# Kernel tuning notes

Measured on AMD Instinct MI355X. Metric: run time of the kernel, lower is better.

Reference implementation:

```python
import jax, jax.numpy as jnp
import numpy as np

N_NODES = 50000
N_EDGES = 800000
N_SUPPORTS = 3
F_IN = 128
F_OUT = 128
BATCH = 1


def _spmm(rows_k, cols_k, vals_k, sup, n_nodes):
    # sup: [B, N, F] dense features; sparse adj given as COO (rows, cols, vals)
    # out[b, r, :] += vals * sup[b, c, :]
    gathered = sup[:, cols_k, :] * vals_k[None, :, None]  # [B, E, F]
    seg = jax.vmap(lambda g: jax.ops.segment_sum(g, rows_k, num_segments=n_nodes))
    return seg(gathered)  # [B, N, F]


def setup_inputs() -> dict:
    key = jax.random.key(0)
    k1, k2, k3, k4, k5 = jax.random.split(key, 5)
    x = jax.random.normal(k1, (BATCH, N_NODES, F_IN), dtype=jnp.float32)
    rows = jax.random.randint(k2, (N_SUPPORTS, N_EDGES), 0, N_NODES)
    cols = jax.random.randint(k3, (N_SUPPORTS, N_EDGES), 0, N_NODES)
    vals = jax.random.uniform(k4, (N_SUPPORTS, N_EDGES), dtype=jnp.float32)
    kernels = jax.random.normal(k5, (N_SUPPORTS, F_IN, F_OUT), dtype=jnp.float32) * (2.0 / (F_IN + F_OUT)) ** 0.5
    bias = jnp.zeros((F_OUT,), dtype=jnp.float32)
    return {"x": x, "rows": rows, "cols": cols, "vals": vals, "kernels": kernels, "bias": bias}


def reference(x, rows, cols, vals, kernels, bias):
    n_nodes = x.shape[1]
    out = None
    for k in range(kernels.shape[0]):  # small fixed number of Chebyshev supports
        sup = jnp.einsum('bnf,fo->bno', x, kernels[k])  # dense feature transform
        acc = _spmm(rows[k], cols[k], vals[k], sup, n_nodes)
        out = acc if out is None else out + acc
    out = out + bias  # bias broadcast over [B, N, F_OUT]
    return jax.nn.relu(out)
```

## Files before the change

### kernel.cpp

```cpp
#include <hip/hip_runtime.h>

#define N_NODES 50000
#define N_EDGES 800000
#define N_SUP   3
#define FD      128
#define NP_PAD  50176

#define NB      196
#define RPB     256
#define EPB     3125
#define NBLK_E  256

typedef __attribute__((ext_vector_type(8))) short bf16x8;
typedef __attribute__((ext_vector_type(4))) float f32x4;

__device__ __forceinline__ unsigned rtn_bf16(float f) {
    unsigned u = __float_as_uint(f);
    return (u + 0x7FFFu + ((u >> 16) & 1u)) >> 16;
}
__device__ __forceinline__ float bf_lo(unsigned g) { return __uint_as_float(g << 16); }
__device__ __forceinline__ float bf_hi(unsigned g) { return __uint_as_float(g & 0xFFFF0000u); }

__global__ __launch_bounds__(256) void cvt_x_kernel(const float4* __restrict__ x4,
                                                    uint2* __restrict__ xb) {
    int i = blockIdx.x * 256 + threadIdx.x;
    if (i >= N_NODES * 32) return;
    float4 v = x4[i];
    xb[i] = make_uint2(rtn_bf16(v.x) | (rtn_bf16(v.y) << 16),
                       rtn_bf16(v.z) | (rtn_bf16(v.w) << 16));
}

__global__ __launch_bounds__(256) void cvt_w_kernel(const float* __restrict__ W,
                                                    uint4* __restrict__ wtb) {
    int tid = blockIdx.x * 256 + threadIdx.x;
    if (tid >= 128 * 48) return;
    int col = tid / 48, p = tid % 48;
    int qlog = (p & ~3) | ((p & 3) ^ ((col >> 1) & 3));
    int k0 = qlog * 8;
    unsigned w0 = rtn_bf16(W[(k0 + 0) * 128 + col]) | (rtn_bf16(W[(k0 + 1) * 128 + col]) << 16);
    unsigned w1 = rtn_bf16(W[(k0 + 2) * 128 + col]) | (rtn_bf16(W[(k0 + 3) * 128 + col]) << 16);
    unsigned w2 = rtn_bf16(W[(k0 + 4) * 128 + col]) | (rtn_bf16(W[(k0 + 5) * 128 + col]) << 16);
    unsigned w3 = rtn_bf16(W[(k0 + 6) * 128 + col]) | (rtn_bf16(W[(k0 + 7) * 128 + col]) << 16);
    wtb[col * 48 + p] = make_uint4(w0, w1, w2, w3);
}

__global__ __launch_bounds__(256) void bhist_kernel(const int* __restrict__ rows,
                                                    int* __restrict__ ghist) {
    __shared__ int hist[NB];
    int t = threadIdx.x, y = blockIdx.y, blk = blockIdx.x;
    for (int i = t; i < NB; i += 256) hist[i] = 0;
    __syncthreads();
    size_t ebase = (size_t)y * N_EDGES + (size_t)blk * EPB;
    for (int i = t; i < EPB; i += 256)
        atomicAdd(&hist[rows[ebase + i] >> 8], 1);
    __syncthreads();
    for (int i = t; i < NB; i += 256)
        if (hist[i]) atomicAdd(&ghist[y * NB + i], hist[i]);
}

__global__ __launch_bounds__(256) void bscan_kernel(const int* __restrict__ ghist,
                                                    int* __restrict__ bucket_start,
                                                    int* __restrict__ gcur) {
    __shared__ int s[256];
    int t = threadIdx.x, y = blockIdx.y;
    int cnt = (t < NB) ? ghist[y * NB + t] : 0;
    int val = cnt;
    s[t] = val; __syncthreads();
    for (int off = 1; off < 256; off <<= 1) {
        int v = (t >= off) ? s[t - off] : 0;
        __syncthreads();
        val += v; s[t] = val;
        __syncthreads();
    }
    int excl = val - cnt;
    if (t < NB) { bucket_start[y * (NB + 1) + t] = excl; gcur[y * NB + t] = excl; }
    if (t == NB - 1) bucket_start[y * (NB + 1) + NB] = val;
}

__global__ __launch_bounds__(256) void part_kernel(const int* __restrict__ rows,
                                                   const int* __restrict__ cols,
                                                   const float* __restrict__ vals,
                                                   int* __restrict__ gcur,
                                                   int2* __restrict__ tmp) {
    __shared__ int2          eS[EPB];
    __shared__ unsigned      packed[EPB];
    __shared__ unsigned char bS[EPB];
    __shared__ int hist[NB], lstart[NB], lcur[NB], gbase[NB];
    __shared__ int s[256];

    int t = threadIdx.x, y = blockIdx.y, blk = blockIdx.x;
    size_t ebase = (size_t)y * N_EDGES + (size_t)blk * EPB;

    for (int i = t; i < NB; i += 256) hist[i] = 0;
    __syncthreads();
    for (int i = t; i < EPB; i += 256) {
        int r = rows[ebase + i];
        int c = cols[ebase + i];
        float v = vals[ebase + i];
        eS[i] = make_int2(c | ((r & 255) << 16), __float_as_int(v));
        bS[i] = (unsigned char)(r >> 8);
        atomicAdd(&hist[r >> 8], 1);
    }
    __syncthreads();

    int cnt = (t < NB) ? hist[t] : 0;
    int val = cnt;
    s[t] = val; __syncthreads();
    for (int off = 1; off < 256; off <<= 1) {
        int v = (t >= off) ? s[t - off] : 0;
        __syncthreads();
        val += v; s[t] = val;
        __syncthreads();
    }
    if (t < NB) {
        int excl = val - cnt;
        lstart[t] = excl; lcur[t] = excl;
        if (cnt > 0) gbase[t] = atomicAdd(&gcur[y * NB + t], cnt);
    }
    __syncthreads();

    for (int i = t; i < EPB; i += 256) {
        int b = bS[i];
        int pos = atomicAdd(&lcur[b], 1);
        packed[pos] = ((unsigned)b << 16) | (unsigned)i;
    }
    __syncthreads();

    for (int i = t; i < EPB; i += 256) {
        unsigned p = packed[i];
        int b = p >> 16, idx = p & 0xFFFF;
        tmp[(size_t)y * N_EDGES + gbase[b] + (i - lstart[b])] = eS[idx];
    }
}

__global__ __launch_bounds__(256) void rowsort_kernel(const int2* __restrict__ tmp,
                                                      const int* __restrict__ bucket_start,
                                                      int2* __restrict__ payload,
                                                      int* __restrict__ row_start) {
    __shared__ int rhist[RPB], rcur[RPB];
    __shared__ int s[256];

    int t = threadIdx.x, b = blockIdx.x, y = blockIdx.y;
    int start = bucket_start[y * (NB + 1) + b];
    int end   = bucket_start[y * (NB + 1) + b + 1];
    int cnt   = end - start;

    rhist[t] = 0;
    __syncthreads();
    const int2* src = tmp + (size_t)y * N_EDGES + start;
    for (int i = t; i < cnt; i += 256)
        atomicAdd(&rhist[((unsigned)src[i].x) >> 16], 1);
    __syncthreads();

    int c0 = rhist[t];
    int val = c0;
    s[t] = val; __syncthreads();
    for (int off = 1; off < 256; off <<= 1) {
        int v = (t >= off) ? s[t - off] : 0;
        __syncthreads();
        val += v; s[t] = val;
        __syncthreads();
    }
    int excl = val - c0;
    rcur[t] = excl;
    int grow = b * RPB + t;
    if (grow < N_NODES) row_start[y * NP_PAD + grow] = start + excl;
    if (b == NB - 1 && t == 0) row_start[y * NP_PAD + N_NODES] = N_EDGES;
    __syncthreads();

    int2* dst = payload + (size_t)y * N_EDGES + start;
    for (int i = t; i < cnt; i += 256) {
        int2 e = src[i];
        int pos = atomicAdd(&rcur[((unsigned)e.x) >> 16], 1);
        dst[pos] = make_int2(e.x & 0xFFFF, e.y);
    }
}

__global__ __launch_bounds__(256) void gather_kernel(const uint4* __restrict__ xb4,
                                                     const int2* __restrict__ payload,
                                                     const int* __restrict__ row_start,
                                                     uint4* __restrict__ zb4) {
    int wid  = threadIdx.x >> 6;
    int lane = threadIdx.x & 63;
    int grp  = lane >> 4;
    int l16  = lane & 15;
    int r = blockIdx.x * 4 + wid;
    if (r >= N_NODES) return;

    const int*  rs  = row_start + blockIdx.y * NP_PAD;
    const int2* pay = payload + (size_t)blockIdx.y * N_EDGES;
    int s = rs[r];
    int e = rs[r + 1];

    float a0 = 0.f, a1 = 0.f, a2 = 0.f, a3 = 0.f;
    float a4 = 0.f, a5 = 0.f, a6 = 0.f, a7 = 0.f;

    int i = s;
    for (; i + 16 <= e; i += 16) {
        int2 pA = pay[i + grp];
        int2 pB = pay[i + 4 + grp];
        int2 pC = pay[i + 8 + grp];
        int2 pD = pay[i + 12 + grp];
        uint4 gA = xb4[(size_t)pA.x * 16 + l16];
        uint4 gB = xb4[(size_t)pB.x * 16 + l16];
        uint4 gC = xb4[(size_t)pC.x * 16 + l16];
        uint4 gD = xb4[(size_t)pD.x * 16 + l16];
        float vA = __int_as_float(pA.y), vB = __int_as_float(pB.y);
        float vC = __int_as_float(pC.y), vD = __int_as_float(pD.y);
        a0 = fmaf(vA, bf_lo(gA.x), a0); a1 = fmaf(vA, bf_hi(gA.x), a1);
        a2 = fmaf(vA, bf_lo(gA.y), a2); a3 = fmaf(vA, bf_hi(gA.y), a3);
        a4 = fmaf(vA, bf_lo(gA.z), a4); a5 = fmaf(vA, bf_hi(gA.z), a5);
        a6 = fmaf(vA, bf_lo(gA.w), a6); a7 = fmaf(vA, bf_hi(gA.w), a7);
        a0 = fmaf(vB, bf_lo(gB.x), a0); a1 = fmaf(vB, bf_hi(gB.x), a1);
        a2 = fmaf(vB, bf_lo(gB.y), a2); a3 = fmaf(vB, bf_hi(gB.y), a3);
        a4 = fmaf(vB, bf_lo(gB.z), a4); a5 = fmaf(vB, bf_hi(gB.z), a5);
        a6 = fmaf(vB, bf_lo(gB.w), a6); a7 = fmaf(vB, bf_hi(gB.w), a7);
        a0 = fmaf(vC, bf_lo(gC.x), a0); a1 = fmaf(vC, bf_hi(gC.x), a1);
        a2 = fmaf(vC, bf_lo(gC.y), a2); a3 = fmaf(vC, bf_hi(gC.y), a3);
        a4 = fmaf(vC, bf_lo(gC.z), a4); a5 = fmaf(vC, bf_hi(gC.z), a5);
        a6 = fmaf(vC, bf_lo(gC.w), a6); a7 = fmaf(vC, bf_hi(gC.w), a7);
        a0 = fmaf(vD, bf_lo(gD.x), a0); a1 = fmaf(vD, bf_hi(gD.x), a1);
        a2 = fmaf(vD, bf_lo(gD.y), a2); a3 = fmaf(vD, bf_hi(gD.y), a3);
        a4 = fmaf(vD, bf_lo(gD.z), a4); a5 = fmaf(vD, bf_hi(gD.z), a5);
        a6 = fmaf(vD, bf_lo(gD.w), a6); a7 = fmaf(vD, bf_hi(gD.w), a7);
    }
    for (; i + 8 <= e; i += 8) {
        int2 pA = pay[i + grp];
        int2 pB = pay[i + 4 + grp];
        uint4 gA = xb4[(size_t)pA.x * 16 + l16];
        uint4 gB = xb4[(size_t)pB.x * 16 + l16];
        float vA = __int_as_float(pA.y), vB = __int_as_float(pB.y);
        a0 = fmaf(vA, bf_lo(gA.x), a0); a1 = fmaf(vA, bf_hi(gA.x), a1);
        a2 = fmaf(vA, bf_lo(gA.y), a2); a3 = fmaf(vA, bf_hi(gA.y), a3);
        a4 = fmaf(vA, bf_lo(gA.z), a4); a5 = fmaf(vA, bf_hi(gA.z), a5);
        a6 = fmaf(vA, bf_lo(gA.w), a6); a7 = fmaf(vA, bf_hi(gA.w), a7);
        a0 = fmaf(vB, bf_lo(gB.x), a0); a1 = fmaf(vB, bf_hi(gB.x), a1);
        a2 = fmaf(vB, bf_lo(gB.y), a2); a3 = fmaf(vB, bf_hi(gB.y), a3);
        a4 = fmaf(vB, bf_lo(gB.z), a4); a5 = fmaf(vB, bf_hi(gB.z), a5);
        a6 = fmaf(vB, bf_lo(gB.w), a6); a7 = fmaf(vB, bf_hi(gB.w), a7);
    }
    for (; i < e; i += 4) {
        int idx = i + grp;
        if (idx < e) {
            int2 p = pay[idx];
            uint4 g = xb4[(size_t)p.x * 16 + l16];
            float v = __int_as_float(p.y);
            a0 = fmaf(v, bf_lo(g.x), a0); a1 = fmaf(v, bf_hi(g.x), a1);
            a2 = fmaf(v, bf_lo(g.y), a2); a3 = fmaf(v, bf_hi(g.y), a3);
            a4 = fmaf(v, bf_lo(g.z), a4); a5 = fmaf(v, bf_hi(g.z), a5);
            a6 = fmaf(v, bf_lo(g.w), a6); a7 = fmaf(v, bf_hi(g.w), a7);
        }
    }

    a0 += __shfl_xor(a0, 16); a0 += __shfl_xor(a0, 32);
    a1 += __shfl_xor(a1, 16); a1 += __shfl_xor(a1, 32);
    a2 += __shfl_xor(a2, 16); a2 += __shfl_xor(a2, 32);
    a3 += __shfl_xor(a3, 16); a3 += __shfl_xor(a3, 32);
    a4 += __shfl_xor(a4, 16); a4 += __shfl_xor(a4, 32);
    a5 += __shfl_xor(a5, 16); a5 += __shfl_xor(a5, 32);
    a6 += __shfl_xor(a6, 16); a6 += __shfl_xor(a6, 32);
    a7 += __shfl_xor(a7, 16); a7 += __shfl_xor(a7, 32);

    if (grp == 0) {
        unsigned q = ((unsigned)(r >> 1)) & 3u;
        uint4 o = make_uint4(rtn_bf16(a0) | (rtn_bf16(a1) << 16),
                             rtn_bf16(a2) | (rtn_bf16(a3) << 16),
                             rtn_bf16(a4) | (rtn_bf16(a5) << 16),
                             rtn_bf16(a6) | (rtn_bf16(a7) << 16));
        zb4[(size_t)r * 48 + blockIdx.y * 16 + (l16 ^ q)] = o;
    }
}

__global__ __launch_bounds__(256) void mfma_gemm_kernel(const char* __restrict__ zb_sw,
                                                        const char* __restrict__ wtb_sw,
                                                        const float* __restrict__ bias,
                                                        float* __restrict__ out) {
    __shared__ __align__(16) char zS[2048];
    __shared__ __align__(16) char wS[8192];

    const int t    = threadIdx.x;
    const int lane = t & 63;
    const int wv   = t >> 6;
    const int row0 = blockIdx.x * 32;
    const int m = lane >> 4;
    const int n = lane & 15;

    const int ar0   = n;
    const int ar1   = 16 + n;
    const int aoff0 = ar0 * 64 + ((m ^ ((ar0 >> 1) & 3)) * 16);
    const int aoff1 = ar1 * 64 + ((m ^ ((ar1 >> 1) & 3)) * 16);
    const int col0  = wv * 32 + n;
    const int col1  = col0 + 16;
    const int boff0 = col0 * 64 + ((m ^ ((col0 >> 1) & 3)) * 16);
    const int boff1 = col1 * 64 + ((m ^ ((col1 >> 1) & 3)) * 16);

    f32x4 acc00 = {0.f, 0.f, 0.f, 0.f};
    f32x4 acc01 = acc00, acc10 = acc00, acc11 = acc00;

    for (int ks = 0; ks < 12; ++ks) {
        __syncthreads();
        if (t < 128) {
            const char* asrc = zb_sw + (size_t)(row0 + (t >> 2)) * 768 + ks * 64 + (t & 3) * 16;
            __builtin_amdgcn_global_load_lds(
                (const __attribute__((address_space(1))) void*)asrc,
                (__attribute__((address_space(3))) void*)(zS + t * 16), 16, 0, 0);
        }
        {
            const char* bsrc0 = wtb_sw + (t >> 2) * 768 + ks * 64 + (t & 3) * 16;
            __builtin_amdgcn_global_load_lds(
                (const __attribute__((address_space(1))) void*)bsrc0,
                (__attribute__((address_space(3))) void*)(wS + t * 16), 16, 0, 0);
            int i = t + 256;
            const char* bsrc1 = wtb_sw + (i >> 2) * 768 + ks * 64 + (i & 3) * 16;
            __builtin_amdgcn_global_load_lds(
                (const __attribute__((address_space(1))) void*)bsrc1,
                (__attribute__((address_space(3))) void*)(wS + i * 16), 16, 0, 0);
        }
        __syncthreads();

        bf16x8 a0 = *(const bf16x8*)(zS + aoff0);
        bf16x8 a1 = *(const bf16x8*)(zS + aoff1);
        bf16x8 b0 = *(const bf16x8*)(wS + boff0);
        bf16x8 b1 = *(const bf16x8*)(wS + boff1);
        acc00 = __builtin_amdgcn_mfma_f32_16x16x32_bf16(a0, b0, acc00, 0, 0, 0);
        acc01 = __builtin_amdgcn_mfma_f32_16x16x32_bf16(a0, b1, acc01, 0, 0, 0);
        acc10 = __builtin_amdgcn_mfma_f32_16x16x32_bf16(a1, b0, acc10, 0, 0, 0);
        acc11 = __builtin_amdgcn_mfma_f32_16x16x32_bf16(a1, b1, acc11, 0, 0, 0);
    }

    float bv0 = bias[col0], bv1 = bias[col1];
    #pragma unroll
    for (int j = 0; j < 4; ++j) {
        int r0 = row0 + m * 4 + j;
        int r1 = r0 + 16;
        if (r0 < N_NODES) {
            out[(size_t)r0 * 128 + col0] = fmaxf(acc00[j] + bv0, 0.f);
            out[(size_t)r0 * 128 + col1] = fmaxf(acc01[j] + bv1, 0.f);
        }
        if (r1 < N_NODES) {
            out[(size_t)r1 * 128 + col0] = fmaxf(acc10[j] + bv0, 0.f);
            out[(size_t)r1 * 128 + col1] = fmaxf(acc11[j] + bv1, 0.f);
        }
    }
}

extern "C" void kernel_launch(void* const* d_in, const int* in_sizes, int n_in,
                              void* d_out, int out_size, void* d_ws, size_t ws_size,
                              hipStream_t stream) {
    const float* x    = (const float*)d_in[0];
    const int*   rows = (const int*)d_in[1];
    const int*   cols = (const int*)d_in[2];
    const float* vals = (const float*)d_in[3];
    const float* kern = (const float*)d_in[4];
    const float* bias = (const float*)d_in[5];
    float* out = (float*)d_out;
    char* ws = (char*)d_ws;

    const size_t OFF_ZB  = 0;
    const size_t OFF_XB  = 38400000;
    const size_t OFF_PAY = OFF_XB + 12800000;
    const size_t OFF_RS  = OFF_PAY + (size_t)N_SUP * N_EDGES * 8;
    const size_t OFF_GH  = OFF_RS + (size_t)N_SUP * NP_PAD * 4;
    const size_t OFF_GC  = OFF_GH + 2368;
    const size_t OFF_BS  = OFF_GC + 2368;
    const size_t OFF_WT  = OFF_BS + 2368;

    unsigned* zb           = (unsigned*)(ws + OFF_ZB);
    int2*     tmp          = (int2*)    (ws + OFF_ZB);
    unsigned* xbuf         = (unsigned*)(ws + OFF_XB);
    int2*     payload      = (int2*)    (ws + OFF_PAY);
    int*      row_start    = (int*)     (ws + OFF_RS);
    int*      ghist        = (int*)     (ws + OFF_GH);
    int*      gcur         = (int*)     (ws + OFF_GC);
    int*      bucket_start = (int*)     (ws + OFF_BS);
    uint4*    wtb          = (uint4*)   (ws + OFF_WT);

    const int row_blocks  = (N_NODES + 3) / 4;
    const int gemm_blocks = (N_NODES + 31) / 32;

    hipMemsetAsync(ghist, 0, N_SUP * NB * 4, stream);
    cvt_x_kernel<<<(N_NODES * 32 + 255) / 256, 256, 0, stream>>>(
        (const float4*)x, (uint2*)xbuf);
    cvt_w_kernel<<<(128 * 48 + 255) / 256, 256, 0, stream>>>(kern, wtb);
    bhist_kernel<<<dim3(NBLK_E, N_SUP), 256, 0, stream>>>(rows, ghist);
    bscan_kernel<<<dim3(1, N_SUP), 256, 0, stream>>>(ghist, bucket_start, gcur);
    part_kernel<<<dim3(NBLK_E, N_SUP), 256, 0, stream>>>(rows, cols, vals, gcur, tmp);
    rowsort_kernel<<<dim3(NB, N_SUP), 256, 0, stream>>>(tmp, bucket_start,
                                                        payload, row_start);
    gather_kernel<<<dim3(row_blocks, N_SUP), 256, 0, stream>>>(
        (const uint4*)xbuf, payload, row_start, (uint4*)zb);
    mfma_gemm_kernel<<<gemm_blocks, 256, 0, stream>>>(
        (const char*)zb, (const char*)wtb, bias, out);
}
```

Before: 255.4 us.

## Replace bucket histogram and scan with fixed-capacity buckets; fuse conversion kernels

```diff
diff --git a/kernel.cpp b/kernel.cpp
--- a/kernel.cpp
+++ b/kernel.cpp
@@ -10,6 +10,7 @@
 #define RPB     256
 #define EPB     3125
 #define NBLK_E  256
+#define CAP     4864
 
 typedef __attribute__((ext_vector_type(8))) short bf16x8;
 typedef __attribute__((ext_vector_type(4))) float f32x4;
@@ -21,66 +22,34 @@
 __device__ __forceinline__ float bf_lo(unsigned g) { return __uint_as_float(g << 16); }
 __device__ __forceinline__ float bf_hi(unsigned g) { return __uint_as_float(g & 0xFFFF0000u); }
 
-__global__ __launch_bounds__(256) void cvt_x_kernel(const float4* __restrict__ x4,
-                                                    uint2* __restrict__ xb) {
-    int i = blockIdx.x * 256 + threadIdx.x;
-    if (i >= N_NODES * 32) return;
-    float4 v = x4[i];
-    xb[i] = make_uint2(rtn_bf16(v.x) | (rtn_bf16(v.y) << 16),
-                       rtn_bf16(v.z) | (rtn_bf16(v.w) << 16));
-}
-
-__global__ __launch_bounds__(256) void cvt_w_kernel(const float* __restrict__ W,
-                                                    uint4* __restrict__ wtb) {
-    int tid = blockIdx.x * 256 + threadIdx.x;
-    if (tid >= 128 * 48) return;
-    int col = tid / 48, p = tid % 48;
-    int qlog = (p & ~3) | ((p & 3) ^ ((col >> 1) & 3));
-    int k0 = qlog * 8;
-    unsigned w0 = rtn_bf16(W[(k0 + 0) * 128 + col]) | (rtn_bf16(W[(k0 + 1) * 128 + col]) << 16);
-    unsigned w1 = rtn_bf16(W[(k0 + 2) * 128 + col]) | (rtn_bf16(W[(k0 + 3) * 128 + col]) << 16);
-    unsigned w2 = rtn_bf16(W[(k0 + 4) * 128 + col]) | (rtn_bf16(W[(k0 + 5) * 128 + col]) << 16);
-    unsigned w3 = rtn_bf16(W[(k0 + 6) * 128 + col]) | (rtn_bf16(W[(k0 + 7) * 128 + col]) << 16);
-    wtb[col * 48 + p] = make_uint4(w0, w1, w2, w3);
-}
-
-__global__ __launch_bounds__(256) void bhist_kernel(const int* __restrict__ rows,
-                                                    int* __restrict__ ghist) {
-    __shared__ int hist[NB];
-    int t = threadIdx.x, y = blockIdx.y, blk = blockIdx.x;
-    for (int i = t; i < NB; i += 256) hist[i] = 0;
-    __syncthreads();
-    size_t ebase = (size_t)y * N_EDGES + (size_t)blk * EPB;
-    for (int i = t; i < EPB; i += 256)
-        atomicAdd(&hist[rows[ebase + i] >> 8], 1);
-    __syncthreads();
-    for (int i = t; i < NB; i += 256)
-        if (hist[i]) atomicAdd(&ghist[y * NB + i], hist[i]);
-}
-
-__global__ __launch_bounds__(256) void bscan_kernel(const int* __restrict__ ghist,
-                                                    int* __restrict__ bucket_start,
-                                                    int* __restrict__ gcur) {
-    __shared__ int s[256];
-    int t = threadIdx.x, y = blockIdx.y;
-    int cnt = (t < NB) ? ghist[y * NB + t] : 0;
-    int val = cnt;
-    s[t] = val; __syncthreads();
-    for (int off = 1; off < 256; off <<= 1) {
-        int v = (t >= off) ? s[t - off] : 0;
-        __syncthreads();
-        val += v; s[t] = val;
-        __syncthreads();
-    }
-    int excl = val - cnt;
-    if (t < NB) { bucket_start[y * (NB + 1) + t] = excl; gcur[y * NB + t] = excl; }
-    if (t == NB - 1) bucket_start[y * (NB + 1) + NB] = val;
+__global__ __launch_bounds__(256) void cvt_xw_kernel(const float4* __restrict__ x4,
+                                                     uint2* __restrict__ xb,
+                                                     const float* __restrict__ W,
+                                                     uint4* __restrict__ wtb) {
+    if (blockIdx.x < 6250) {
+        int i = blockIdx.x * 256 + threadIdx.x;
+        if (i >= N_NODES * 32) return;
+        float4 v = x4[i];
+        xb[i] = make_uint2(rtn_bf16(v.x) | (rtn_bf16(v.y) << 16),
+                           rtn_bf16(v.z) | (rtn_bf16(v.w) << 16));
+    } else {
+        int tid = (blockIdx.x - 6250) * 256 + threadIdx.x;
+        if (tid >= 128 * 48) return;
+        int col = tid / 48, p = tid % 48;
+        int qlog = (p & ~3) | ((p & 3) ^ ((col >> 1) & 3));
+        int k0 = qlog * 8;
+        unsigned w0 = rtn_bf16(W[(k0 + 0) * 128 + col]) | (rtn_bf16(W[(k0 + 1) * 128 + col]) << 16);
+        unsigned w1 = rtn_bf16(W[(k0 + 2) * 128 + col]) | (rtn_bf16(W[(k0 + 3) * 128 + col]) << 16);
+        unsigned w2 = rtn_bf16(W[(k0 + 4) * 128 + col]) | (rtn_bf16(W[(k0 + 5) * 128 + col]) << 16);
+        unsigned w3 = rtn_bf16(W[(k0 + 6) * 128 + col]) | (rtn_bf16(W[(k0 + 7) * 128 + col]) << 16);
+        wtb[col * 48 + p] = make_uint4(w0, w1, w2, w3);
+    }
 }
 
 __global__ __launch_bounds__(256) void part_kernel(const int* __restrict__ rows,
                                                    const int* __restrict__ cols,
                                                    const float* __restrict__ vals,
-                                                   int* __restrict__ gcur,
+                                                   int* __restrict__ gcount,
                                                    int2* __restrict__ tmp) {
     __shared__ int2          eS[EPB];
     __shared__ unsigned      packed[EPB];
@@ -115,7 +84,8 @@
     if (t < NB) {
         int excl = val - cnt;
         lstart[t] = excl; lcur[t] = excl;
-        if (cnt > 0) gbase[t] = atomicAdd(&gcur[y * NB + t], cnt);
+        if (cnt > 0)
+            gbase[t] = t * CAP + atomicAdd(&gcount[y * NB + t], cnt);
     }
     __syncthreads();
 
@@ -129,25 +99,23 @@
     for (int i = t; i < EPB; i += 256) {
         unsigned p = packed[i];
         int b = p >> 16, idx = p & 0xFFFF;
-        tmp[(size_t)y * N_EDGES + gbase[b] + (i - lstart[b])] = eS[idx];
+        tmp[(size_t)y * (NB * CAP) + gbase[b] + (i - lstart[b])] = eS[idx];
     }
 }
 
 __global__ __launch_bounds__(256) void rowsort_kernel(const int2* __restrict__ tmp,
-                                                      const int* __restrict__ bucket_start,
+                                                      const int* __restrict__ gcount,
                                                       int2* __restrict__ payload,
                                                       int* __restrict__ row_start) {
     __shared__ int rhist[RPB], rcur[RPB];
     __shared__ int s[256];
 
     int t = threadIdx.x, b = blockIdx.x, y = blockIdx.y;
-    int start = bucket_start[y * (NB + 1) + b];
-    int end   = bucket_start[y * (NB + 1) + b + 1];
-    int cnt   = end - start;
+    int cnt = gcount[y * NB + b];
 
     rhist[t] = 0;
     __syncthreads();
-    const int2* src = tmp + (size_t)y * N_EDGES + start;
+    const int2* src = tmp + (size_t)y * (NB * CAP) + (size_t)b * CAP;
     for (int i = t; i < cnt; i += 256)
         atomicAdd(&rhist[((unsigned)src[i].x) >> 16], 1);
     __syncthreads();
@@ -164,16 +132,19 @@
     int excl = val - c0;
     rcur[t] = excl;
     int grow = b * RPB + t;
-    if (grow < N_NODES) row_start[y * NP_PAD + grow] = start + excl;
-    if (b == NB - 1 && t == 0) row_start[y * NP_PAD + N_NODES] = N_EDGES;
-    __syncthreads();
-
-    int2* dst = payload + (size_t)y * N_EDGES + start;
+    if (grow < N_NODES) row_start[y * NP_PAD + grow] = b * CAP + excl;
+    if (b == NB - 1 && t == 0)
+        row_start[y * NP_PAD + N_NODES] = (NB - 1) * CAP + cnt;
+    __syncthreads();
+
+    int2* dst = payload + (size_t)y * (NB * CAP) + (size_t)b * CAP;
     for (int i = t; i < cnt; i += 256) {
         int2 e = src[i];
         int pos = atomicAdd(&rcur[((unsigned)e.x) >> 16], 1);
         dst[pos] = make_int2(e.x & 0xFFFF, e.y);
     }
+    for (int i = cnt + t; i < CAP; i += 256)
+        dst[i] = make_int2(0, 0);
 }
 
 __global__ __launch_bounds__(256) void gather_kernel(const uint4* __restrict__ xb4,
@@ -188,7 +159,7 @@
     if (r >= N_NODES) return;
 
     const int*  rs  = row_start + blockIdx.y * NP_PAD;
-    const int2* pay = payload + (size_t)blockIdx.y * N_EDGES;
+    const int2* pay = payload + (size_t)blockIdx.y * (NB * CAP);
     int s = rs[r];
     int e = rs[r + 1];
 
@@ -356,36 +327,31 @@
     float* out = (float*)d_out;
     char* ws = (char*)d_ws;
 
+    const size_t SLOT    = (size_t)NB * CAP;
     const size_t OFF_ZB  = 0;
     const size_t OFF_XB  = 38400000;
     const size_t OFF_PAY = OFF_XB + 12800000;
-    const size_t OFF_RS  = OFF_PAY + (size_t)N_SUP * N_EDGES * 8;
-    const size_t OFF_GH  = OFF_RS + (size_t)N_SUP * NP_PAD * 4;
-    const size_t OFF_GC  = OFF_GH + 2368;
-    const size_t OFF_BS  = OFF_GC + 2368;
-    const size_t OFF_WT  = OFF_BS + 2368;
-
-    unsigned* zb           = (unsigned*)(ws + OFF_ZB);
-    int2*     tmp          = (int2*)    (ws + OFF_ZB);
-    unsigned* xbuf         = (unsigned*)(ws + OFF_XB);
-    int2*     payload      = (int2*)    (ws + OFF_PAY);
-    int*      row_start    = (int*)     (ws + OFF_RS);
-    int*      ghist        = (int*)     (ws + OFF_GH);
-    int*      gcur         = (int*)     (ws + OFF_GC);
-    int*      bucket_start = (int*)     (ws + OFF_BS);
-    uint4*    wtb          = (uint4*)   (ws + OFF_WT);
+    const size_t OFF_RS  = OFF_PAY + (size_t)N_SUP * SLOT * 8;
+    const size_t OFF_GC  = OFF_RS + (size_t)N_SUP * NP_PAD * 4;
+    const size_t OFF_WT  = OFF_GC + 2368;
+
+    unsigned* zb        = (unsigned*)(ws + OFF_ZB);
+    int2*     tmp       = (int2*)    (ws + OFF_ZB);
+    unsigned* xbuf      = (unsigned*)(ws + OFF_XB);
+    int2*     payload   = (int2*)    (ws + OFF_PAY);
+    int*      row_start = (int*)     (ws + OFF_RS);
+    int*      gcount    = (int*)     (ws + OFF_GC);
+    uint4*    wtb       = (uint4*)   (ws + OFF_WT);
 
     const int row_blocks  = (N_NODES + 3) / 4;
     const int gemm_blocks = (N_NODES + 31) / 32;
 
-    hipMemsetAsync(ghist, 0, N_SUP * NB * 4, stream);
-    cvt_x_kernel<<<(N_NODES * 32 + 255) / 256, 256, 0, stream>>>(
-        (const float4*)x, (uint2*)xbuf);
-    cvt_w_kernel<<<(128 * 48 + 255) / 256, 256, 0, stream>>>(kern, wtb);
-    bhist_kernel<<<dim3(NBLK_E, N_SUP), 256, 0, stream>>>(rows, ghist);
-    bscan_kernel<<<dim3(1, N_SUP), 256, 0, stream>>>(ghist, bucket_start, gcur);
-    part_kernel<<<dim3(NBLK_E, N_SUP), 256, 0, stream>>>(rows, cols, vals, gcur, tmp);
-    rowsort_kernel<<<dim3(NB, N_SUP), 256, 0, stream>>>(tmp, bucket_start,
+    hipMemsetAsync(gcount, 0, N_SUP * NB * 4, stream);
+    cvt_xw_kernel<<<6250 + 24, 256, 0, stream>>>(
+        (const float4*)x, (uint2*)xbuf, kern, wtb);
+    part_kernel<<<dim3(NBLK_E, N_SUP), 256, 0, stream>>>(rows, cols, vals,
+                                                         gcount, tmp);
+    rowsort_kernel<<<dim3(NB, N_SUP), 256, 0, stream>>>(tmp, gcount,
                                                         payload, row_start);
     gather_kernel<<<dim3(row_blocks, N_SUP), 256, 0, stream>>>(
         (const uint4*)xbuf, payload, row_start, (uint4*)zb);
```

Result: slower. 364.9 us (+42.9%).
